# Performance work log

Hardware: AMD Instinct MI355X
Metric: run time of the kernel (lower is better)

## Reference

```python
import jax, jax.numpy as jnp
import numpy as np

D = 1024      # model_dim (input_dim)
H = 2048      # hidden_size_per_expert (hardcoded in module)
E = 8         # num_experts
K = 2         # topk
T = 8192      # tokens (batch after view)


def setup_inputs() -> dict:
    key = jax.random.key(0)
    ks = jax.random.split(key, 6)
    s_in = 1.0 / np.sqrt(D)
    s_h = 1.0 / np.sqrt(H)
    return {
        "x": jax.random.normal(ks[0], (T, D), dtype=jnp.float32),
        "wg": jax.random.normal(ks[1], (D, E), dtype=jnp.float32) * s_in,   # gate Linear(D,E,bias=False)
        "w1": jax.random.normal(ks[2], (E, D, H), dtype=jnp.float32) * s_in,
        "b1": jnp.zeros((E, H), dtype=jnp.float32),
        "w2": jax.random.normal(ks[3], (E, H, D), dtype=jnp.float32) * s_h,
        "b2": jnp.zeros((E, D), dtype=jnp.float32),
    }


def _moe(x, wg, w1, b1, w2, b2):
    # top-k gating (Tutel 'top' gate, k=K)
    logits = x @ wg                         # [T,E]
    scores = jax.nn.softmax(logits, -1)     # [T,E]
    topv, topi = jax.lax.top_k(scores, K)   # [T,K]
    sel = jax.nn.one_hot(topi, E, dtype=x.dtype)          # [T,K,E]
    combine = jnp.einsum('tk,tke->te', topv, sel)          # sparse combine weights [T,E]
    # GShard-style load-balance aux loss (top-1 dispatch mask)
    ce = sel[:, 0, :].mean(0)               # fraction of tokens whose top1 is e
    me = scores.mean(0)                     # mean gate prob per expert
    l_aux = jnp.sum(me * ce) * E
    # expert FFN (dense over experts; combine zeros out non-selected)
    h = jax.nn.relu(jnp.einsum('td,edh->teh', x, w1) + b1)  # [T,E,H]
    y = jnp.einsum('teh,ehd->ted', h, w2) + b2              # [T,E,D]
    out = jnp.einsum('te,ted->td', combine, y)              # [T,D]
    return out, l_aux


def reference(x, wg, w1, b1, w2, b2):
    return _moe(x, wg, w1, b1, w2, b2)
```

## Files before the change

kernel.cpp:

```cpp
#include <hip/hip_runtime.h>
#include <stdint.h>

#define T_TOK 8192
#define DIM   1024
#define HID   2048
#define NE    8

#define BM 128
#define BN 128
#define BK 64

#define GB_TOK 32

typedef float floatx4 __attribute__((ext_vector_type(4)));
typedef short shortx8 __attribute__((ext_vector_type(8)));

typedef __attribute__((address_space(3))) void       lds_void;
typedef const __attribute__((address_space(1))) void gbl_void;

__device__ __forceinline__ unsigned short f2bf(float f) {
  unsigned int u = __float_as_uint(f);
  unsigned int r = 0x7fffu + ((u >> 16) & 1u);
  return (unsigned short)((u + r) >> 16);
}

__global__ __launch_bounds__(256) void cast_x_kernel(const float* __restrict__ x,
                                                     unsigned short* __restrict__ xb) {
  size_t i = ((size_t)blockIdx.x * 256 + threadIdx.x) * 4;
  float4 v = *reinterpret_cast<const float4*>(x + i);
  ushort4 o;
  o.x = f2bf(v.x); o.y = f2bf(v.y); o.z = f2bf(v.z); o.w = f2bf(v.w);
  *reinterpret_cast<ushort4*>(xb + i) = o;
}

__global__ __launch_bounds__(256) void transpose_cast_kernel(const float* __restrict__ in,
                                                             unsigned short* __restrict__ out,
                                                             int R, int C) {
  __shared__ float tile[32][33];
  const size_t eoff = (size_t)blockIdx.z * R * C;
  const float* ip = in + eoff;
  unsigned short* op = out + eoff;
  int c0 = blockIdx.x * 32, r0 = blockIdx.y * 32;
  int tx = threadIdx.x, ty = threadIdx.y;
#pragma unroll
  for (int i = 0; i < 4; i++)
    tile[ty + i * 8][tx] = ip[(size_t)(r0 + ty + i * 8) * C + (c0 + tx)];
  __syncthreads();
#pragma unroll
  for (int i = 0; i < 4; i++)
    op[(size_t)(c0 + ty + i * 8) * R + (r0 + tx)] = f2bf(tile[tx][ty + i * 8]);
}

__global__ __launch_bounds__(256) void gate_kernel(const float* __restrict__ x,
                                                   const float* __restrict__ wg,
                                                   int* counts, int* top1cnt, float* ssum,
                                                   int* tok_list, float* wgt_list) {
  __shared__ int   lds_cnt[8];
  __shared__ int   lds_top1[8];
  __shared__ float lds_ssum[4][8];
  __shared__ int   tk_e[GB_TOK][2];
  __shared__ int   tk_r[GB_TOK][2];
  __shared__ float tk_w[GB_TOK][2];
  __shared__ int   base[8];

  const int tid = threadIdx.x;
  const int wave = tid >> 6;
  const int lane = tid & 63;

  if (tid < 8) { lds_cnt[tid] = 0; lds_top1[tid] = 0; }
  if (tid < 32) lds_ssum[tid >> 3][tid & 7] = 0.f;
  __syncthreads();

  float ssum_local[8];
#pragma unroll
  for (int e = 0; e < 8; e++) ssum_local[e] = 0.f;

  for (int it = 0; it < GB_TOK / 4; it++) {
    const int lt = it * 4 + wave;
    const int t = blockIdx.x * GB_TOK + lt;

    float acc[8];
#pragma unroll
    for (int e = 0; e < 8; e++) acc[e] = 0.f;
    const float* xr = x + (size_t)t * DIM;
#pragma unroll
    for (int i = 0; i < 16; i++) {
      int d = i * 64 + lane;
      float xv = xr[d];
      const float4* wr = reinterpret_cast<const float4*>(wg + d * 8);
      float4 w0 = wr[0], w1 = wr[1];
      acc[0] += xv * w0.x; acc[1] += xv * w0.y; acc[2] += xv * w0.z; acc[3] += xv * w0.w;
      acc[4] += xv * w1.x; acc[5] += xv * w1.y; acc[6] += xv * w1.z; acc[7] += xv * w1.w;
    }
#pragma unroll
    for (int e = 0; e < 8; e++) {
#pragma unroll
      for (int off = 32; off > 0; off >>= 1) acc[e] += __shfl_xor(acc[e], off, 64);
    }
    if (lane == 0) {
      float mx = acc[0];
#pragma unroll
      for (int e = 1; e < 8; e++) mx = fmaxf(mx, acc[e]);
      float s[8], sum = 0.f;
#pragma unroll
      for (int e = 0; e < 8; e++) { s[e] = expf(acc[e] - mx); sum += s[e]; }
      float inv = 1.f / sum;
#pragma unroll
      for (int e = 0; e < 8; e++) { s[e] *= inv; ssum_local[e] += s[e]; }
      int i1 = 0;
#pragma unroll
      for (int e = 1; e < 8; e++) if (s[e] > s[i1]) i1 = e;
      int i2 = (i1 == 0) ? 1 : 0;
#pragma unroll
      for (int e = 0; e < 8; e++) if (e != i1 && s[e] > s[i2]) i2 = e;
      atomicAdd(&lds_top1[i1], 1);
      int r1 = atomicAdd(&lds_cnt[i1], 1);
      int r2 = atomicAdd(&lds_cnt[i2], 1);
      tk_e[lt][0] = i1; tk_r[lt][0] = r1; tk_w[lt][0] = s[i1];
      tk_e[lt][1] = i2; tk_r[lt][1] = r2; tk_w[lt][1] = s[i2];
    }
  }
  if (lane == 0) {
#pragma unroll
    for (int e = 0; e < 8; e++) lds_ssum[wave][e] = ssum_local[e];
  }
  __syncthreads();
  if (tid < 8) {
    base[tid] = atomicAdd(&counts[tid], lds_cnt[tid]);
    atomicAdd(&top1cnt[tid], lds_top1[tid]);
    atomicAdd(&ssum[tid],
              lds_ssum[0][tid] + lds_ssum[1][tid] + lds_ssum[2][tid] + lds_ssum[3][tid]);
  }
  __syncthreads();
  if (tid < GB_TOK * 2) {
    int lt = tid >> 1, k = tid & 1;
    int e = tk_e[lt][k];
    int pos = base[e] + tk_r[lt][k];
    tok_list[e * T_TOK + pos] = blockIdx.x * GB_TOK + lt;
    wgt_list[e * T_TOK + pos] = tk_w[lt][k];
  }
}

__global__ void scan_kernel(const int* counts, const int* top1cnt, const float* ssum,
                            int* h_off, float* laux_out) {
  if (threadIdx.x == 0 && blockIdx.x == 0) {
    int off = 0;
    float l = 0.f;
    for (int e = 0; e < 8; e++) {
      h_off[e] = off;
      off += counts[e];
      l += (ssum[e] / (float)T_TOK) * ((float)top1cnt[e] / (float)T_TOK);
    }
    *laux_out = l * (float)NE;
  }
}

template <int MODE>
__global__ __launch_bounds__(256, 4) void moe_gemm_kernel(
    const unsigned short* __restrict__ A_src, const unsigned short* __restrict__ B_src,
    const float* __restrict__ bias, const int* __restrict__ counts,
    const int* __restrict__ h_off, const int* __restrict__ tok_list,
    const float* __restrict__ wgt_list, unsigned short* __restrict__ h_out,
    float* __restrict__ out, int N, int K) {
  __shared__ unsigned short s_a[BM][BK];
  __shared__ unsigned short s_b[BN][BK];

  const int e = blockIdx.z;
  const int n_e = counts[e];
  const int m0 = blockIdx.y * BM;
  if (m0 >= n_e) return;
  const int n0 = blockIdx.x * BN;
  const int tid = threadIdx.x;

  const int lane = tid & 63;
  const int wv = tid >> 6;
  const int lrow = lane >> 3;
  const int lchk = (lane & 7) ^ lrow;

  const unsigned short* a_g[4];
  const unsigned short* b_g[4];
  lds_void* a_l[4];
  lds_void* b_l[4];
#pragma unroll
  for (int c = 0; c < 4; c++) {
    int ra = wv * 32 + c * 8 + lrow;
    int gr = m0 + ra;
    int safe = (gr < n_e) ? gr : (n_e - 1);
    const unsigned short* abase;
    if (MODE == 0) {
      int tok = tok_list[e * T_TOK + safe];
      abase = A_src + (size_t)tok * K;
    } else {
      abase = A_src + (size_t)(h_off[e] + safe) * K;
    }
    a_g[c] = abase + lchk * 8;
    b_g[c] = B_src + ((size_t)e * N + n0 + ra) * K + lchk * 8;
    a_l[c] = (lds_void*)&s_a[wv * 32 + c * 8][0];
    b_l[c] = (lds_void*)&s_b[wv * 32 + c * 8][0];
  }

  const int lm = lane & 15;
  const int quad = lane >> 4;
  const int r7 = lm & 7;
  const int wm = (wv >> 1) * 64;
  const int wn = (wv & 1) * 64;

  floatx4 acc[4][4];
#pragma unroll
  for (int mi = 0; mi < 4; mi++)
#pragma unroll
    for (int ni = 0; ni < 4; ni++) acc[mi][ni] = (floatx4){0.f, 0.f, 0.f, 0.f};

  for (int kt = 0; kt < K; kt += BK) {
#pragma unroll
    for (int c = 0; c < 4; c++) {
      __builtin_amdgcn_global_load_lds((gbl_void*)(a_g[c] + kt), a_l[c], 16, 0, 0);
      __builtin_amdgcn_global_load_lds((gbl_void*)(b_g[c] + kt), b_l[c], 16, 0, 0);
    }
    __syncthreads();
#pragma unroll
    for (int kk = 0; kk < 2; kk++) {
      const int pc = ((kk << 2) + quad) ^ r7;
      shortx8 af[4], bfr[4];
#pragma unroll
      for (int mi = 0; mi < 4; mi++)
        af[mi] = *reinterpret_cast<const shortx8*>(&s_a[wm + mi * 16 + lm][pc << 3]);
#pragma unroll
      for (int ni = 0; ni < 4; ni++)
        bfr[ni] = *reinterpret_cast<const shortx8*>(&s_b[wn + ni * 16 + lm][pc << 3]);
#pragma unroll
      for (int mi = 0; mi < 4; mi++)
#pragma unroll
        for (int ni = 0; ni < 4; ni++)
          acc[mi][ni] = __builtin_amdgcn_mfma_f32_16x16x32_bf16(af[mi], bfr[ni], acc[mi][ni], 0, 0, 0);
    }
    __syncthreads();
  }

#pragma unroll
  for (int mi = 0; mi < 4; mi++) {
#pragma unroll
    for (int r = 0; r < 4; r++) {
      int row = m0 + wm + mi * 16 + quad * 4 + r;
      if (row >= n_e) continue;
      if (MODE == 0) {
        size_t base = (size_t)(h_off[e] + row) * N;
#pragma unroll
        for (int ni = 0; ni < 4; ni++) {
          int col = n0 + wn + ni * 16 + lm;
          float v = acc[mi][ni][r] + bias[e * N + col];
          v = fmaxf(v, 0.f);
          h_out[base + col] = f2bf(v);
        }
      } else {
        int tok = tok_list[e * T_TOK + row];
        float wgt = wgt_list[e * T_TOK + row];
        size_t base = (size_t)tok * N;
#pragma unroll
        for (int ni = 0; ni < 4; ni++) {
          int col = n0 + wn + ni * 16 + lm;
          float v = wgt * (acc[mi][ni][r] + bias[e * N + col]);
          atomicAdd(&out[base + col], v);
        }
      }
    }
  }
}

extern "C" void kernel_launch(void* const* d_in, const int* in_sizes, int n_in,
                              void* d_out, int out_size, void* d_ws, size_t ws_size,
                              hipStream_t stream) {
  const float* x  = (const float*)d_in[0];
  const float* wg = (const float*)d_in[1];
  const float* w1 = (const float*)d_in[2];
  const float* b1 = (const float*)d_in[3];
  const float* w2 = (const float*)d_in[4];
  const float* b2 = (const float*)d_in[5];
  float* out = (float*)d_out;

  char* ws = (char*)d_ws;
  int*            counts   = (int*)(ws + 0);
  int*            top1cnt  = (int*)(ws + 32);
  float*          ssum     = (float*)(ws + 64);
  int*            h_off    = (int*)(ws + 96);
  int*            tok_list = (int*)(ws + 256);
  float*          wgt_list = (float*)(ws + 262400);
  unsigned short* x_bf     = (unsigned short*)(ws + 524544);
  unsigned short* w1t      = (unsigned short*)(ws + 17301760);
  unsigned short* w2t      = (unsigned short*)(ws + 50856192);
  unsigned short* h_buf    = (unsigned short*)(ws + 84410624);

  hipMemsetAsync(ws, 0, 256, stream);
  hipMemsetAsync(d_out, 0, (size_t)out_size * sizeof(float), stream);

  cast_x_kernel<<<(T_TOK * DIM) / 1024, 256, 0, stream>>>(x, x_bf);

  dim3 tb(32, 8);
  transpose_cast_kernel<<<dim3(HID / 32, DIM / 32, NE), tb, 0, stream>>>(w1, w1t, DIM, HID);
  transpose_cast_kernel<<<dim3(DIM / 32, HID / 32, NE), tb, 0, stream>>>(w2, w2t, HID, DIM);

  gate_kernel<<<T_TOK / GB_TOK, 256, 0, stream>>>(x, wg, counts, top1cnt, ssum, tok_list, wgt_list);
  scan_kernel<<<1, 64, 0, stream>>>(counts, top1cnt, ssum, h_off, out + (size_t)T_TOK * DIM);

  moe_gemm_kernel<0><<<dim3(HID / BN, T_TOK / BM, NE), 256, 0, stream>>>(
      x_bf, w1t, b1, counts, h_off, tok_list, wgt_list, h_buf, nullptr, HID, DIM);
  moe_gemm_kernel<1><<<dim3(DIM / BN, T_TOK / BM, NE), 256, 0, stream>>>(
      h_buf, w2t, b2, counts, h_off, tok_list, wgt_list, nullptr, out, DIM, HID);
}
```

Measured before the change: 490.7 us.

## Double-buffer GEMM K-tiles with async LDS loads and fuse x cast into gate

Rewrites the expert GEMM main loop to hold two LDS buffers with BK=32. The next tile is prefetched by global_load_lds while the current one feeds the MFMAs, with explicit vmcnt waits and barriers in place of the load-sync-compute pattern. The LDS swizzle changes to match the narrower tile. The x-to-bf16 cast is also folded into the gate kernel, which already reads x, removing one kernel launch and one extra read of x. The smaller K-tile means more iterations and barriers per tile, and the gate kernel now writes bf16 scalars uncoalesced in 2-byte units.

```diff
diff --git a/kernel.cpp b/kernel.cpp
--- a/kernel.cpp
+++ b/kernel.cpp
@@ -8,7 +8,7 @@
 
 #define BM 128
 #define BN 128
-#define BK 64
+#define BK2 32
 
 #define GB_TOK 32
 
@@ -22,15 +22,6 @@
   unsigned int u = __float_as_uint(f);
   unsigned int r = 0x7fffu + ((u >> 16) & 1u);
   return (unsigned short)((u + r) >> 16);
-}
-
-__global__ __launch_bounds__(256) void cast_x_kernel(const float* __restrict__ x,
-                                                     unsigned short* __restrict__ xb) {
-  size_t i = ((size_t)blockIdx.x * 256 + threadIdx.x) * 4;
-  float4 v = *reinterpret_cast<const float4*>(x + i);
-  ushort4 o;
-  o.x = f2bf(v.x); o.y = f2bf(v.y); o.z = f2bf(v.z); o.w = f2bf(v.w);
-  *reinterpret_cast<ushort4*>(xb + i) = o;
 }
 
 __global__ __launch_bounds__(256) void transpose_cast_kernel(const float* __restrict__ in,
@@ -53,6 +44,7 @@
 
 __global__ __launch_bounds__(256) void gate_kernel(const float* __restrict__ x,
                                                    const float* __restrict__ wg,
+                                                   unsigned short* __restrict__ x_bf,
                                                    int* counts, int* top1cnt, float* ssum,
                                                    int* tok_list, float* wgt_list) {
   __shared__ int   lds_cnt[8];
@@ -83,10 +75,12 @@
 #pragma unroll
     for (int e = 0; e < 8; e++) acc[e] = 0.f;
     const float* xr = x + (size_t)t * DIM;
+    unsigned short* xbr = x_bf + (size_t)t * DIM;
 #pragma unroll
     for (int i = 0; i < 16; i++) {
       int d = i * 64 + lane;
       float xv = xr[d];
+      xbr[d] = f2bf(xv);
       const float4* wr = reinterpret_cast<const float4*>(wg + d * 8);
       float4 w0 = wr[0], w1 = wr[1];
       acc[0] += xv * w0.x; acc[1] += xv * w0.y; acc[2] += xv * w0.z; acc[3] += xv * w0.w;
@@ -162,8 +156,8 @@
     const int* __restrict__ h_off, const int* __restrict__ tok_list,
     const float* __restrict__ wgt_list, unsigned short* __restrict__ h_out,
     float* __restrict__ out, int N, int K) {
-  __shared__ unsigned short s_a[BM][BK];
-  __shared__ unsigned short s_b[BN][BK];
+  __shared__ unsigned short s_a[2][BM][BK2];
+  __shared__ unsigned short s_b[2][BN][BK2];
 
   const int e = blockIdx.z;
   const int n_e = counts[e];
@@ -174,16 +168,15 @@
 
   const int lane = tid & 63;
   const int wv = tid >> 6;
-  const int lrow = lane >> 3;
-  const int lchk = (lane & 7) ^ lrow;
-
-  const unsigned short* a_g[4];
-  const unsigned short* b_g[4];
-  lds_void* a_l[4];
-  lds_void* b_l[4];
-#pragma unroll
-  for (int c = 0; c < 4; c++) {
-    int ra = wv * 32 + c * 8 + lrow;
+
+  const int srow = (lane >> 2);
+  const int gchk = (lane & 3) ^ ((lane >> 3) & 3);
+
+  const unsigned short* a_g[2];
+  const unsigned short* b_g[2];
+#pragma unroll
+  for (int c = 0; c < 2; c++) {
+    int ra = c * 64 + wv * 16 + srow;
     int gr = m0 + ra;
     int safe = (gr < n_e) ? gr : (n_e - 1);
     const unsigned short* abase;
@@ -193,15 +186,13 @@
     } else {
       abase = A_src + (size_t)(h_off[e] + safe) * K;
     }
-    a_g[c] = abase + lchk * 8;
-    b_g[c] = B_src + ((size_t)e * N + n0 + ra) * K + lchk * 8;
-    a_l[c] = (lds_void*)&s_a[wv * 32 + c * 8][0];
-    b_l[c] = (lds_void*)&s_b[wv * 32 + c * 8][0];
+    a_g[c] = abase + gchk * 8;
+    b_g[c] = B_src + ((size_t)e * N + n0 + ra) * K + gchk * 8;
   }
 
   const int lm = lane & 15;
   const int quad = lane >> 4;
-  const int r7 = lm & 7;
+  const int pchk = quad ^ ((lm >> 1) & 3);
   const int wm = (wv >> 1) * 64;
   const int wn = (wv & 1) * 64;
 
@@ -211,30 +202,43 @@
 #pragma unroll
     for (int ni = 0; ni < 4; ni++) acc[mi][ni] = (floatx4){0.f, 0.f, 0.f, 0.f};
 
-  for (int kt = 0; kt < K; kt += BK) {
-#pragma unroll
-    for (int c = 0; c < 4; c++) {
-      __builtin_amdgcn_global_load_lds((gbl_void*)(a_g[c] + kt), a_l[c], 16, 0, 0);
-      __builtin_amdgcn_global_load_lds((gbl_void*)(b_g[c] + kt), b_l[c], 16, 0, 0);
-    }
-    __syncthreads();
-#pragma unroll
-    for (int kk = 0; kk < 2; kk++) {
-      const int pc = ((kk << 2) + quad) ^ r7;
-      shortx8 af[4], bfr[4];
-#pragma unroll
-      for (int mi = 0; mi < 4; mi++)
-        af[mi] = *reinterpret_cast<const shortx8*>(&s_a[wm + mi * 16 + lm][pc << 3]);
+  const int nk = K / BK2;
+
+#pragma unroll
+  for (int c = 0; c < 2; c++) {
+    __builtin_amdgcn_global_load_lds((gbl_void*)a_g[c], (lds_void*)&s_a[0][c * 64 + wv * 16][0], 16, 0, 0);
+    __builtin_amdgcn_global_load_lds((gbl_void*)b_g[c], (lds_void*)&s_b[0][c * 64 + wv * 16][0], 16, 0, 0);
+  }
+
+  for (int kt = 0; kt < nk; kt++) {
+    const int cur = kt & 1;
+    if (kt + 1 < nk) {
+      const int nxt = cur ^ 1;
+      const int ko = (kt + 1) * BK2;
+#pragma unroll
+      for (int c = 0; c < 2; c++) {
+        __builtin_amdgcn_global_load_lds((gbl_void*)(a_g[c] + ko), (lds_void*)&s_a[nxt][c * 64 + wv * 16][0], 16, 0, 0);
+        __builtin_amdgcn_global_load_lds((gbl_void*)(b_g[c] + ko), (lds_void*)&s_b[nxt][c * 64 + wv * 16][0], 16, 0, 0);
+      }
+      asm volatile("s_waitcnt vmcnt(4)\n\ts_barrier" ::: "memory");
+    } else {
+      asm volatile("s_waitcnt vmcnt(0)\n\ts_barrier" ::: "memory");
+    }
+
+    shortx8 af[4], bfr[4];
+#pragma unroll
+    for (int mi = 0; mi < 4; mi++)
+      af[mi] = *reinterpret_cast<const shortx8*>(&s_a[cur][wm + mi * 16 + lm][pchk << 3]);
+#pragma unroll
+    for (int ni = 0; ni < 4; ni++)
+      bfr[ni] = *reinterpret_cast<const shortx8*>(&s_b[cur][wn + ni * 16 + lm][pchk << 3]);
+#pragma unroll
+    for (int mi = 0; mi < 4; mi++)
 #pragma unroll
       for (int ni = 0; ni < 4; ni++)
-        bfr[ni] = *reinterpret_cast<const shortx8*>(&s_b[wn + ni * 16 + lm][pc << 3]);
-#pragma unroll
-      for (int mi = 0; mi < 4; mi++)
-#pragma unroll
-        for (int ni = 0; ni < 4; ni++)
-          acc[mi][ni] = __builtin_amdgcn_mfma_f32_16x16x32_bf16(af[mi], bfr[ni], acc[mi][ni], 0, 0, 0);
-    }
-    __syncthreads();
+        acc[mi][ni] = __builtin_amdgcn_mfma_f32_16x16x32_bf16(af[mi], bfr[ni], acc[mi][ni], 0, 0, 0);
+
+    asm volatile("s_barrier" ::: "memory");
   }
 
 #pragma unroll
@@ -293,17 +297,15 @@
   hipMemsetAsync(ws, 0, 256, stream);
   hipMemsetAsync(d_out, 0, (size_t)out_size * sizeof(float), stream);
 
-  cast_x_kernel<<<(T_TOK * DIM) / 1024, 256, 0, stream>>>(x, x_bf);
-
   dim3 tb(32, 8);
   transpose_cast_kernel<<<dim3(HID / 32, DIM / 32, NE), tb, 0, stream>>>(w1, w1t, DIM, HID);
   transpose_cast_kernel<<<dim3(DIM / 32, HID / 32, NE), tb, 0, stream>>>(w2, w2t, HID, DIM);
 
-  gate_kernel<<<T_TOK / GB_TOK, 256, 0, stream>>>(x, wg, counts, top1cnt, ssum, tok_list, wgt_list);
+  gate_kernel<<<T_TOK / GB_TOK, 256, 0, stream>>>(x, wg, x_bf, counts, top1cnt, ssum, tok_list, wgt_list);
   scan_kernel<<<1, 64, 0, stream>>>(counts, top1cnt, ssum, h_off, out + (size_t)T_TOK * DIM);
 
-  moe_gemm_kernel<0><<<dim3(HID / BN, T_TOK / BM, NE), 256, 0, stream>>>(
+  moe_gemm_kernel<0><<<dim3(HID / BM, T_TOK / BM, NE), 256, 0, stream>>>(
       x_bf, w1t, b1, counts, h_off, tok_list, wgt_list, h_buf, nullptr, HID, DIM);
-  moe_gemm_kernel<1><<<dim3(DIM / BN, T_TOK / BM, NE), 256, 0, stream>>>(
+  moe_gemm_kernel<1><<<dim3(DIM / BM, T_TOK / BM, NE), 256, 0, stream>>>(
       h_buf, w2t, b2, counts, h_off, tok_list, wgt_list, nullptr, out, DIM, HID);
 }
```

Result: slower. 520.0 us (+6.0%).
